# Kernel tuning notes

Hardware: AMD Instinct MI355X
Metric: run time of the kernel (lower is better)

Reference implementation:

```python
import jax, jax.numpy as jnp
import numpy as np

CD_STEPS = 1

def _sample_binary(p, u):
    # relu(sign(p - u)): 1.0 where p > u else 0.0
    return (p > u).astype(p.dtype)

def setup_inputs() -> dict:
    key = jax.random.key(0)
    k_v, k_w, k_vb, k_uh, k_uv = jax.random.split(key, 5)
    B, V, H = 8192, 2048, 1024
    return {
        "v": jax.random.uniform(k_v, (B, V), dtype=jnp.float32),
        "w": jax.random.normal(k_w, (V, H), dtype=jnp.float32) * 0.01,
        "vb": jax.random.normal(k_vb, (V,), dtype=jnp.float32) * 0.01,
        "hb": jnp.zeros((H,), dtype=jnp.float32),
        "u_h": jax.random.uniform(k_uh, (CD_STEPS + 1, B, H), dtype=jnp.float32),
        "u_v": jax.random.uniform(k_uv, (CD_STEPS, B, V), dtype=jnp.float32),
    }

def reference(v, w, vb, hb, u_h, u_v):
    sig = jax.nn.sigmoid
    # mean-field forward
    h_p = sig(hb + v @ w)                     # [B,H]
    h_prediction = h_p
    v_prediction = sig(vb + h_p @ w.T)        # [B,V]
    reconstruction_error = jnp.mean(jnp.mean(jnp.abs(v - v_prediction), axis=1))
    # data statistics
    h = _sample_binary(h_p, u_h[0])           # [B,H]
    vb_data_grad = jnp.sum(v, axis=0)
    hb_data_grad = jnp.sum(h_p, axis=0)
    # sum_b outer(v_b, h_b) == v^T @ h (original materialized [B,V,H])
    w_data_grad = jnp.einsum('bv,bh->vh', v, h)
    # CD-k chain
    vk = v
    for k in range(CD_STEPS):
        vk = _sample_binary(sig(vb + h @ w.T), u_v[k])
        h = _sample_binary(sig(hb + vk @ w), u_h[k + 1])
    vb_model_grad = jnp.sum(vk, axis=0)
    hb_model_grad = jnp.sum(h, axis=0)
    w_model_grad = jnp.einsum('bv,bh->vh', vk, h)
    vb_grad = vb_model_grad - vb_data_grad
    hb_grad = hb_model_grad - hb_data_grad
    w_grad = w_model_grad - w_data_grad
    return h_prediction, reconstruction_error, w_grad, vb_grad, hb_grad
```

## Files before the change

kernel.cpp:

```cpp
#include <hip/hip_runtime.h>


typedef unsigned short u16;
typedef short s16x8 __attribute__((ext_vector_type(8)));
typedef float f32x4 __attribute__((ext_vector_type(4)));
typedef u16 u16x4 __attribute__((ext_vector_type(4)));
typedef u16 u16x8 __attribute__((ext_vector_type(8)));

constexpr int Bn = 8192, Vn = 2048, Hn = 1024;
constexpr size_t VH = (size_t)Vn * Hn;
constexpr size_t BH = (size_t)Bn * Hn;
constexpr size_t OUT_RECON = BH;
constexpr size_t OUT_WGRAD = OUT_RECON + 1;
constexpr size_t OUT_VBG   = OUT_WGRAD + VH;
constexpr size_t OUT_HBG   = OUT_VBG + Vn;

__device__ __forceinline__ u16 f2bf(float x) {
  union { float f; unsigned u; } a; a.f = x;
  unsigned r = a.u + 0x7FFFu + ((a.u >> 16) & 1u);
  return (u16)(r >> 16);
}
__device__ __forceinline__ float bf2f(u16 h) {
  union { unsigned u; float f; } a; a.u = ((unsigned)h) << 16;
  return a.f;
}
__device__ __forceinline__ float sigmoidf_(float x) {
  return 1.0f / (1.0f + __expf(-x));
}

using gptr_t = const unsigned int __attribute__((address_space(1)))*;
using lptr_t = unsigned int __attribute__((address_space(3)))*;

__device__ __forceinline__ void gload16(const u16* g, u16* l) {
  __builtin_amdgcn_global_load_lds((gptr_t)(unsigned long long)g,
                                   (lptr_t)(unsigned long long)l, 16, 0, 0);
}

__global__ void prep_all_k(const float* __restrict__ v, u16* __restrict__ vcat,
                           u16* __restrict__ vT, float* __restrict__ vbd_p,
                           const float* __restrict__ w, u16* __restrict__ w_cat,
                           u16* __restrict__ wTc) {
  __shared__ u16 tile16[64][68];
  __shared__ float cs[16][64];
  __shared__ float tile32[64][65];
  const int bx = blockIdx.x;
  const int t = threadIdx.x;
  if (bx < 4096) {
    const int b0 = (bx & 127) << 6, c0 = (bx >> 7) << 6;
    const int rg = t >> 4;
    const int cg = (t & 15) << 2;
    float ca[4] = {0.f, 0.f, 0.f, 0.f};
#pragma unroll
    for (int i = 0; i < 4; ++i) {
      int r = rg + 16 * i;
      f32x4 x = *(const f32x4*)&v[(size_t)(b0 + r) * Vn + c0 + cg];
      u16x4 hi, lo;
#pragma unroll
      for (int j = 0; j < 4; ++j) {
        hi[j] = f2bf(x[j]);
        lo[j] = f2bf(x[j] - bf2f(hi[j]));
        tile16[r][cg + j] = hi[j];
        ca[j] += x[j];
      }
      *(u16x4*)&vcat[(size_t)(b0 + r) * (2 * Vn) + c0 + cg] = hi;
      *(u16x4*)&vcat[(size_t)(b0 + r) * (2 * Vn) + Vn + c0 + cg] = lo;
    }
#pragma unroll
    for (int j = 0; j < 4; ++j) cs[rg][cg + j] = ca[j];
    __syncthreads();
    if (t < 64) {
      float s = 0.f;
#pragma unroll
      for (int k = 0; k < 16; ++k) s += cs[k][t];
      vbd_p[(size_t)(bx & 127) * Vn + c0 + t] = s;
    }
#pragma unroll
    for (int s2 = 0; s2 < 2; ++s2) {
      int c = t >> 2;
      int seg = (t & 3) + 4 * s2;
      u16x8 pk;
#pragma unroll
      for (int i = 0; i < 8; ++i) pk[i] = tile16[seg * 8 + i][c];
      *(u16x8*)&vT[(size_t)(c0 + c) * Bn + b0 + seg * 8] = pk;
    }
  } else {
    const int wb = bx - 4096;
    const int v0 = (wb & 31) << 6, h0 = (wb >> 5) << 6;
    const int c = t & 63, r = t >> 6;
    for (int rr = r; rr < 64; rr += 4) {
      float x = w[(size_t)(v0 + rr) * Hn + h0 + c];
      tile32[rr][c] = x;
      u16 hi = f2bf(x), lo = f2bf(x - bf2f(hi));
      w_cat[(size_t)(v0 + rr) * (2 * Hn) + h0 + c]      = hi;
      w_cat[(size_t)(v0 + rr) * (2 * Hn) + Hn + h0 + c] = lo;
    }
    __syncthreads();
    for (int rr = r; rr < 64; rr += 4) {
      float x = tile32[c][rr];
      u16 hi = f2bf(x), lo = f2bf(x - bf2f(hi));
      size_t ro = (size_t)(h0 + rr) * (2 * Vn);
      wTc[ro + v0 + c]      = hi;
      wTc[ro + Vn + v0 + c] = lo;
    }
  }
}

template <int M>
__global__ void epi_h_k(const float* __restrict__ p0, const float* __restrict__ p1,
                        const float* __restrict__ bias, const float* __restrict__ uni,
                        float* __restrict__ f32out, u16* __restrict__ hp_out,
                        u16* __restrict__ hbin_out, u16* __restrict__ tout,
                        float* __restrict__ colp) {
  __shared__ u16 tile[64][68];
  __shared__ float cs[16][64];
  const int b0 = blockIdx.x * 64, c0 = blockIdx.y * 64;
  const int t = threadIdx.x;
  const int rg = t >> 4, cg = (t & 15) << 2;
  float ca[4] = {0.f, 0.f, 0.f, 0.f};
#pragma unroll
  for (int i = 0; i < 4; ++i) {
    int r = rg + 16 * i;
    size_t e = (size_t)(b0 + r) * Hn + c0 + cg;
    f32x4 a = *(const f32x4*)&p0[e];
    f32x4 b = *(const f32x4*)&p1[e];
    f32x4 uu = *(const f32x4*)&uni[e];
    f32x4 hpv;
    u16x4 hb16, qv;
#pragma unroll
    for (int j = 0; j < 4; ++j) {
      float hp = sigmoidf_(a[j] + b[j] + bias[c0 + cg + j]);
      u16 qb = (hp > uu[j]) ? (u16)0x3F80 : (u16)0;
      tile[r][cg + j] = qb;
      if constexpr (M == 1) {
        hpv[j] = hp; hb16[j] = f2bf(hp); qv[j] = qb;
        ca[j] += hp;
      } else {
        ca[j] += (qb ? 1.f : 0.f);
      }
    }
    if constexpr (M == 1) {
      *(f32x4*)&f32out[e] = hpv;
      *(u16x4*)&hp_out[e] = hb16;
      *(u16x4*)&hbin_out[e] = qv;
    }
  }
#pragma unroll
  for (int j = 0; j < 4; ++j) cs[rg][cg + j] = ca[j];
  __syncthreads();
  if (t < 64) {
    float s = 0.f;
#pragma unroll
    for (int k = 0; k < 16; ++k) s += cs[k][t];
    colp[(size_t)blockIdx.x * Hn + c0 + t] = s;
  }
#pragma unroll
  for (int s2 = 0; s2 < 2; ++s2) {
    int c = t >> 2;
    int seg = (t & 3) + 4 * s2;
    u16x8 pk;
#pragma unroll
    for (int i = 0; i < 8; ++i) pk[i] = tile[seg * 8 + i][c];
    *(u16x8*)&tout[(size_t)(c0 + c) * Bn + b0 + seg * 8] = pk;
  }
}

template <int MODE>
__global__ __launch_bounds__(512) void gemm256(
    const u16* __restrict__ A, int lda, const u16* __restrict__ Bm, int ldb, int K,
    const float* __restrict__ bias, const float* __restrict__ uni,
    const float* __restrict__ aux, float* __restrict__ f32out,
    u16* __restrict__ bfout, const u16* __restrict__ aux16,
    float* __restrict__ redp, u16* __restrict__ tout, float* __restrict__ colp) {
  constexpr bool TRANS = (MODE == 4);
  __shared__ __align__(16) u16 smem[TRANS ? 67584 : 65536];
  const int t = threadIdx.x;
  const int lane = t & 63, wave = t >> 6;
  const int wr = (wave >> 2) << 7;
  const int wc = (wave & 3) << 6;
  int bidx = blockIdx.x, bidy = blockIdx.y, bidz = blockIdx.z;
  if constexpr (MODE == 3) {
    const int orig = blockIdx.x + (blockIdx.y << 3) + (blockIdx.z << 5);
    bidz = orig & 7;
    const int r = orig >> 3;
    bidx = r & 7;
    bidy = r >> 3;
  }
  const int bm = bidx << 8, bn = bidy << 8;
  int kbeg = 0;
  float* pout = f32out;
  if constexpr (MODE == 1 || MODE == 5) {
    kbeg = bidz * K;
    pout = (bidz == 0) ? f32out : redp;
  }
  if constexpr (MODE == 3) {
    size_t off = (size_t)bidz * (size_t)K;
    A += off;
    Bm += off;
    pout = ((bidz < 4) ? f32out : redp) + (size_t)(bidz & 3) * VH;
  }
  f32x4 acc[8][4] = {};
  const int sr = t >> 2;
  const int sc = (((t & 3) ^ ((t >> 3) & 3)) << 3);
  const u16* Ag  = A  + (size_t)(bm + sr) * lda + sc;
  const u16* Ag2 = Ag + (size_t)128 * lda;
  const u16* Bg  = Bm + (size_t)(bn + sr) * ldb + sc;
  const u16* Bg2 = Bg + (size_t)128 * ldb;
  const int fr = lane & 15, fg = lane >> 4;
  const int ga = ((fg ^ ((fr >> 1) & 3)) << 3);

  auto acolf = [&](int k0) -> int {
    if constexpr (MODE == 1)      return (k0 < 2048) ? k0 : k0 - 2048;
    else if constexpr (MODE == 4) return k0 & 1023;
    else if constexpr (MODE == 5) return k0 & 2047;
    else                          return k0;
  };
  auto bcolf = [&](int k0) -> int {
    if constexpr (MODE == 1) return (k0 < 4096) ? k0 : k0 - 4096;
    else                     return k0;
  };
  auto stageA = [&](int kt) {
    const int k0 = kbeg + (kt << 5);
    const int acol = acolf(k0);
    u16* ad = smem + (kt & 3) * 8192 + wave * 512;
    gload16(Ag + acol, ad);
    gload16(Ag2 + acol, ad + 4096);
  };
  auto stageB = [&](int kt) {
    const int k0 = kbeg + (kt << 5);
    const int bcol = bcolf(k0);
    u16* bd = smem + 32768 + (kt & 3) * 8192 + wave * 512;
    gload16(Bg + bcol, bd);
    gload16(Bg2 + bcol, bd + 4096);
  };
  auto pfl4 = [&](int ci) -> float {
    const int L = (ci << 9) + t;
    return uni[(size_t)(bm + (L >> 3)) * Vn + bn + ((L & 7) << 5)];
  };

  const int NT = K >> 5;
  const int pfbeg = NT - 8;
  stageA(0); stageB(0); stageA(1); stageB(1); stageA(2); stageB(2);
  asm volatile("s_waitcnt vmcnt(8)" ::: "memory");
  __builtin_amdgcn_s_barrier();
  asm volatile("" ::: "memory");
  s16x8 bf[4], af[4];
  for (int kt = 0; kt < NT; ++kt) {
    const int pb = kt & 3;
    const u16* Ab = smem + pb * 8192;
    const u16* Bb = smem + 32768 + pb * 8192;
    const bool st = (kt < NT - 3);
#pragma unroll
    for (int n = 0; n < 4; ++n)
      bf[n] = *(const s16x8*)&Bb[(wc + n * 16 + fr) * 32 + ga];
#pragma unroll
    for (int m = 0; m < 4; ++m)
      af[m] = *(const s16x8*)&Ab[(wr + m * 16 + fr) * 32 + ga];
    if (st) stageA(kt + 3);
    if constexpr (MODE == 4) {
      if (kt >= pfbeg && kt < pfbeg + 4) {
        float pfv = pfl4(kt - pfbeg);
        asm volatile("" :: "v"(pfv));
      }
    }
    __builtin_amdgcn_s_barrier();
    asm volatile("" ::: "memory");
    __builtin_amdgcn_s_setprio(1);
#pragma unroll
    for (int m = 0; m < 4; ++m)
#pragma unroll
      for (int n = 0; n < 4; ++n)
        acc[m][n] = __builtin_amdgcn_mfma_f32_16x16x32_bf16(af[m], bf[n], acc[m][n], 0, 0, 0);
    __builtin_amdgcn_s_setprio(0);
#pragma unroll
    for (int m = 0; m < 4; ++m)
      af[m] = *(const s16x8*)&Ab[(wr + (m + 4) * 16 + fr) * 32 + ga];
    if (st) stageB(kt + 3);
    if (kt < NT - 3) {
      asm volatile("s_waitcnt vmcnt(8)" ::: "memory");
    } else if (kt == NT - 3) {
      asm volatile("s_waitcnt vmcnt(4)" ::: "memory");
    } else if (kt == NT - 2) {
      asm volatile("s_waitcnt vmcnt(0)" ::: "memory");
    }
    __builtin_amdgcn_s_barrier();
    asm volatile("" ::: "memory");
    __builtin_amdgcn_s_setprio(1);
#pragma unroll
    for (int m = 0; m < 4; ++m)
#pragma unroll
      for (int n = 0; n < 4; ++n)
        acc[m + 4][n] = __builtin_amdgcn_mfma_f32_16x16x32_bf16(af[m], bf[n], acc[m + 4][n], 0, 0, 0);
    __builtin_amdgcn_s_setprio(0);
  }

  constexpr int NC = (MODE == 4) ? Vn : Hn;
  const int fq = lane >> 4;

  if constexpr (MODE == 1 || MODE == 3 || MODE == 5) {
#pragma unroll
    for (int m = 0; m < 8; ++m)
#pragma unroll
      for (int n = 0; n < 4; ++n)
#pragma unroll
        for (int j = 0; j < 4; ++j) {
          int rl = wr + m * 16 + fq * 4 + j;
          int cl = wc + n * 16 + fr;
          pout[(size_t)(bm + rl) * NC + bn + cl] = acc[m][n][j];
        }
  }

  if constexpr (MODE == 4) {
    __syncthreads();
    float bcol[4];
#pragma unroll
    for (int n = 0; n < 4; ++n) bcol[n] = bias[bn + wc + n * 16 + fr];
    const size_t ebase = (size_t)(bm + wr + fq * 4) * NC + (bn + wc + fr);
    float ux[8][4];
    auto ld4 = [&](int ci, float* dst) {
      size_t e0 = ebase + (size_t)((ci >> 2) << 4) * NC + ((ci & 3) << 4);
      dst[0] = uni[e0];          dst[1] = uni[e0 + NC];
      dst[2] = uni[e0 + 2 * NC]; dst[3] = uni[e0 + 3 * NC];
    };
#pragma unroll
    for (int ci = 0; ci < 8; ++ci) ld4(ci, ux[ci]);
#pragma unroll
    for (int m = 0; m < 8; ++m)
#pragma unroll
      for (int n = 0; n < 4; ++n)
#pragma unroll
        for (int j = 0; j < 4; ++j)
          acc[m][n][j] = sigmoidf_(acc[m][n][j] + bcol[n]);
    float csum[4] = {0.f, 0.f, 0.f, 0.f};
#pragma unroll
    for (int ci = 0; ci < 32; ++ci) {
      const int m = ci >> 2, n = ci & 3;
      const int rl = wr + m * 16 + fq * 4;
      const int cl = wc + n * 16 + fr;
#pragma unroll
      for (int j = 0; j < 4; ++j) {
        u16 qb = (acc[m][n][j] > ux[ci & 7][j]) ? (u16)0x3F80 : (u16)0;
        smem[(rl + j) * 264 + cl] = qb;
        csum[n] += (qb ? 1.f : 0.f);
      }
      if (ci < 24) ld4(ci + 8, ux[ci & 7]);
    }
#pragma unroll
    for (int n = 0; n < 4; ++n) {
      float s = csum[n];
      s += __shfl_xor(s, 16);
      s += __shfl_xor(s, 32);
      if (fq == 0)
        colp[(size_t)(blockIdx.x * 2 + (wr >> 7)) * NC + (bn + wc + n * 16 + fr)] = s;
    }
    __syncthreads();
#pragma unroll
    for (int it = 0; it < 16; ++it) {
      int id = t + (it << 9);
      int r = id >> 5;
      int c0 = (id & 31) << 3;
      u16x8 pk = *(const u16x8*)&smem[r * 264 + c0];
      *(u16x8*)&bfout[(size_t)(bm + r) * NC + bn + c0] = pk;
    }
#pragma unroll
    for (int it = 0; it < 4; ++it) {
      int id = t + (it << 9);
      int c = id & 255;
      int q = id >> 8;
#pragma unroll
      for (int i8 = 0; i8 < 4; ++i8) {
        u16x8 pk;
#pragma unroll
        for (int i2 = 0; i2 < 8; ++i2)
          pk[i2] = smem[(q * 32 + i8 * 8 + i2) * 264 + c];
        *(u16x8*)&tout[(size_t)(bn + c) * Bn + bm + q * 32 + i8 * 8] = pk;
      }
    }
  }
}

__global__ __launch_bounds__(512) void g23_k(
    const u16* __restrict__ A2, const u16* __restrict__ B2,
    const u16* __restrict__ aux16, const float* __restrict__ bias2,
    float* __restrict__ redp2,
    const u16* __restrict__ A3, const u16* __restrict__ B3,
    float* __restrict__ out30, float* __restrict__ out34) {
  __shared__ __align__(16) u16 smem[65536];
  const int t = threadIdx.x;
  const int lane = t & 63, wave = t >> 6;
  const int wr = (wave >> 2) << 7;
  const int wc = (wave & 3) << 6;
  const int flat = blockIdx.x;
  const bool isG2 = (flat < 256);
  int bidx, bidy, bidz = 0;
  const u16 *Abase, *Bbase;
  int lda, ldb;
  if (isG2) {
    bidx = flat & 31; bidy = flat >> 5;
    Abase = A2; Bbase = B2; lda = Hn; ldb = 2 * Hn;
  } else {
    const int orig = flat - 256;
    bidz = orig & 7;
    const int rr = orig >> 3;
    bidx = rr & 7; bidy = rr >> 3;
    Abase = A3 + (size_t)bidz * 1024;
    Bbase = B3 + (size_t)bidz * 1024;
    lda = Bn; ldb = Bn;
  }
  const int bm = bidx << 8, bn = bidy << 8;
  f32x4 acc[8][4] = {};
  const int sr = t >> 2;
  const int sc = (((t & 3) ^ ((t >> 3) & 3)) << 3);
  const u16* Ag  = Abase + (size_t)(bm + sr) * lda + sc;
  const u16* Ag2 = Ag + (size_t)128 * lda;
  const u16* Bg  = Bbase + (size_t)(bn + sr) * ldb + sc;
  const u16* Bg2 = Bg + (size_t)128 * ldb;
  const int fr = lane & 15, fg = lane >> 4;
  const int ga = ((fg ^ ((fr >> 1) & 3)) << 3);

  auto stageA = [&](int kt) {
    u16* ad = smem + (kt & 3) * 8192 + wave * 512;
    gload16(Ag + (kt << 5), ad);
    gload16(Ag2 + (kt << 5), ad + 4096);
  };
  auto stageB = [&](int kt) {
    u16* bd = smem + 32768 + (kt & 3) * 8192 + wave * 512;
    gload16(Bg + (kt << 5), bd);
    gload16(Bg2 + (kt << 5), bd + 4096);
  };
  auto pfl2 = [&](int ci) -> unsigned {
    const int L = (ci << 9) + t;
    return (unsigned)aux16[(size_t)(bm + (L >> 2)) * 4096 + bn + ((L & 3) << 6)];
  };

  constexpr int NT = 32;
  stageA(0); stageB(0); stageA(1); stageB(1); stageA(2); stageB(2);
  asm volatile("s_waitcnt vmcnt(8)" ::: "memory");
  __builtin_amdgcn_s_barrier();
  asm volatile("" ::: "memory");
  s16x8 bf[4], af[4];
  for (int kt = 0; kt < NT; ++kt) {
    const int pb = kt & 3;
    const u16* Ab = smem + pb * 8192;
    const u16* Bb = smem + 32768 + pb * 8192;
    const bool st = (kt < NT - 3);
#pragma unroll
    for (int n = 0; n < 4; ++n)
      bf[n] = *(const s16x8*)&Bb[(wc + n * 16 + fr) * 32 + ga];
#pragma unroll
    for (int m = 0; m < 4; ++m)
      af[m] = *(const s16x8*)&Ab[(wr + m * 16 + fr) * 32 + ga];
    if (st) stageA(kt + 3);
    if (isG2 && kt >= NT - 8 && kt < NT - 6) {
      unsigned pfv = pfl2(kt - (NT - 8));
      asm volatile("" :: "v"(pfv));
    }
    __builtin_amdgcn_s_barrier();
    asm volatile("" ::: "memory");
    __builtin_amdgcn_s_setprio(1);
#pragma unroll
    for (int m = 0; m < 4; ++m)
#pragma unroll
      for (int n = 0; n < 4; ++n)
        acc[m][n] = __builtin_amdgcn_mfma_f32_16x16x32_bf16(af[m], bf[n], acc[m][n], 0, 0, 0);
    __builtin_amdgcn_s_setprio(0);
#pragma unroll
    for (int m = 0; m < 4; ++m)
      af[m] = *(const s16x8*)&Ab[(wr + (m + 4) * 16 + fr) * 32 + ga];
    if (st) stageB(kt + 3);
    if (kt < NT - 3) {
      asm volatile("s_waitcnt vmcnt(8)" ::: "memory");
    } else if (kt == NT - 3) {
      asm volatile("s_waitcnt vmcnt(4)" ::: "memory");
    } else if (kt == NT - 2) {
      asm volatile("s_waitcnt vmcnt(0)" ::: "memory");
    }
    __builtin_amdgcn_s_barrier();
    asm volatile("" ::: "memory");
    __builtin_amdgcn_s_setprio(1);
#pragma unroll
    for (int m = 0; m < 4; ++m)
#pragma unroll
      for (int n = 0; n < 4; ++n)
        acc[m + 4][n] = __builtin_amdgcn_mfma_f32_16x16x32_bf16(af[m], bf[n], acc[m + 4][n], 0, 0, 0);
    __builtin_amdgcn_s_setprio(0);
  }

  const int fq = lane >> 4;
  if (isG2) {
    float bcol[4];
#pragma unroll
    for (int n = 0; n < 4; ++n) bcol[n] = bias2[bn + wc + n * 16 + fr];
    const size_t ebase = (size_t)(bm + wr + fq * 4) * 4096 + (bn + wc + fr);
    float ax[8][4];
    auto ld4 = [&](int ci, float* dst) {
      size_t e0 = ebase + (size_t)((ci >> 2) << 4) * 4096 + ((ci & 3) << 4);
      dst[0] = bf2f(aux16[e0]);            dst[1] = bf2f(aux16[e0 + 4096]);
      dst[2] = bf2f(aux16[e0 + 2 * 4096]); dst[3] = bf2f(aux16[e0 + 3 * 4096]);
    };
#pragma unroll
    for (int ci = 0; ci < 8; ++ci) ld4(ci, ax[ci]);
#pragma unroll
    for (int m = 0; m < 8; ++m)
#pragma unroll
      for (int n = 0; n < 4; ++n)
#pragma unroll
        for (int j = 0; j < 4; ++j)
          acc[m][n][j] = sigmoidf_(acc[m][n][j] + bcol[n]);
    float lsum = 0.f;
#pragma unroll
    for (int ci = 0; ci < 32; ++ci) {
      const int m = ci >> 2, n = ci & 3;
#pragma unroll
      for (int j = 0; j < 4; ++j) lsum += fabsf(ax[ci & 7][j] - acc[m][n][j]);
      if (ci < 24) ld4(ci + 8, ax[ci & 7]);
    }
#pragma unroll
    for (int off = 32; off > 0; off >>= 1) lsum += __shfl_down(lsum, off);
    __syncthreads();
    float* redlds = (float*)smem;
    if (lane == 0) redlds[wave] = lsum;
    __syncthreads();
    if (t == 0) {
      float s = 0.f;
#pragma unroll
      for (int wv = 0; wv < 8; ++wv) s += redlds[wv];
      redp2[(size_t)bidy * 32 + bidx] = s;
    }
  } else {
    float* pout = ((bidz < 4) ? out30 : out34) + (size_t)(bidz & 3) * VH;
#pragma unroll
    for (int m = 0; m < 8; ++m)
#pragma unroll
      for (int n = 0; n < 4; ++n)
#pragma unroll
        for (int j = 0; j < 4; ++j) {
          int rl = wr + m * 16 + fq * 4 + j;
          int cl = wc + n * 16 + fr;
          pout[(size_t)(bm + rl) * Hn + bn + cl] = acc[m][n][j];
        }
  }
}

__global__ void reduce8_k(const float* __restrict__ p, float* __restrict__ out) {
  size_t e = ((size_t)blockIdx.x * 256 + threadIdx.x) * 4;
  f32x4 r = {};
#pragma unroll
  for (int z = 0; z < 8; ++z) r += *(const f32x4*)&p[(size_t)z * VH + e];
  out[e + 0] = r[0]; out[e + 1] = r[1]; out[e + 2] = r[2]; out[e + 3] = r[3];
}

__global__ void tail_k(const float* __restrict__ pa, const float* __restrict__ pb,
                       const float* __restrict__ sums, float* __restrict__ out) {
  const int b = blockIdx.x;
  float* outw = out + OUT_WGRAD;
  if (b < 2048) {
    size_t e = ((size_t)b * 256 + threadIdx.x) * 4;
    f32x4 r = {};
#pragma unroll
    for (int z = 0; z < 4; ++z) r += *(const f32x4*)&pa[(size_t)z * VH + e];
#pragma unroll
    for (int z = 0; z < 4; ++z) r += *(const f32x4*)&pb[(size_t)z * VH + e];
    float s0 = outw[e + 0], s1 = outw[e + 1], s2 = outw[e + 2], s3 = outw[e + 3];
    outw[e + 0] = r[0] - s0; outw[e + 1] = r[1] - s1;
    outw[e + 2] = r[2] - s2; outw[e + 3] = r[3] - s3;
  } else {
    const int i = (b - 2048) * 256 + threadIdx.x;
    const float* recon_p = sums;
    const float* vbd = sums + 1024;
    const float* hbd = vbd + 128 * 2048;
    const float* vbm = hbd + 128 * 1024;
    const float* hbm = vbm + 128 * 2048;
    if (i < 2048) {
      float d = 0.f, m = 0.f;
      for (int k = 0; k < 128; ++k) d += vbd[k * 2048 + i];
      for (int k = 0; k < 64; ++k)  m += vbm[k * 2048 + i];
      out[OUT_VBG + i] = m - d;
    }
    if (i < 1024) {
      float d = 0.f, m = 0.f;
      for (int k = 0; k < 128; ++k) { d += hbd[k * 1024 + i]; m += hbm[k * 1024 + i]; }
      out[OUT_HBG + i] = m - d;
    }
    if (i == 0) {
      float s = 0.f;
      for (int k = 0; k < 256; ++k) s += recon_p[k];
      out[OUT_RECON] = s * (1.0f / 16777216.0f);
    }
  }
}

extern "C" void kernel_launch(void* const* d_in, const int* in_sizes, int n_in,
                              void* d_out, int out_size, void* d_ws, size_t ws_size,
                              hipStream_t stream) {
  (void)in_sizes; (void)n_in; (void)out_size;
  const float* v   = (const float*)d_in[0];
  const float* w   = (const float*)d_in[1];
  const float* vb  = (const float*)d_in[2];
  const float* hb  = (const float*)d_in[3];
  const float* u_h = (const float*)d_in[4];
  const float* u_v = (const float*)d_in[5];
  float* out = (float*)d_out;
  char* ws = (char*)d_ws;
  if (ws_size < 204734464ULL) return;

  float* sums    = (float*)ws;
  float* recon_p = sums;
  float* vbd_p   = sums + 1024;
  float* hbd_p   = vbd_p + 128 * 2048;
  float* vbm_p   = hbd_p + 128 * 1024;
  float* hbm_p   = vbm_p + 128 * 2048;
  char* p = ws + 3407872;
  u16* v_cat  = (u16*)p;  p += (size_t)Bn * 2 * Vn * 2;
  u16* wT_cat = (u16*)p;  p += (size_t)Hn * 2 * Vn * 2;
  u16* w_cat  = (u16*)p;  p += (size_t)Vn * 2 * Hn * 2;
  u16* h_p    = (u16*)p;  p += BH * 2;
  u16* hbin   = (u16*)p;  p += BH * 2;
  u16* vT     = (u16*)p;  p += (size_t)Vn * Bn * 2;
  u16* hT     = (u16*)p;  p += (size_t)Hn * Bn * 2;
  float* big  = (float*)p;
  u16* vk   = v_cat;
  u16* vkT  = vT;
  u16* h2T  = hT;
  float* vcat_f = (float*)v_cat;
  float* hpbuf  = (float*)h_p;
  float* outW   = out + OUT_WGRAD;

  prep_all_k<<<4608, 256, 0, stream>>>(v, v_cat, vT, vbd_p, w, w_cat, wT_cat);
  gemm256<1><<<dim3(32, 4, 2), 512, 0, stream>>>(
      v_cat, 2 * Vn, wT_cat, 2 * Vn, 3072, nullptr, nullptr, nullptr,
      out, nullptr, nullptr, big, nullptr, nullptr);
  epi_h_k<1><<<dim3(128, 16), 256, 0, stream>>>(
      out, big, hb, u_h, out, h_p, hbin, hT, hbd_p);
  g23_k<<<512, 512, 0, stream>>>(
      h_p, w_cat, v_cat, vb, recon_p,
      vT, hT, vcat_f, vcat_f + 4 * VH);
  reduce8_k<<<2048, 256, 0, stream>>>(vcat_f, outW);
  gemm256<4><<<dim3(32, 8), 512, 0, stream>>>(
      hbin, Hn, w_cat, 2 * Hn, 2 * Hn, vb, u_v, nullptr,
      nullptr, vk, nullptr, nullptr, vkT, vbm_p);
  gemm256<5><<<dim3(32, 4, 2), 512, 0, stream>>>(
      vk, Vn, wT_cat, 2 * Vn, 2048, nullptr, nullptr, nullptr,
      hpbuf, nullptr, nullptr, big, nullptr, nullptr);
  epi_h_k<5><<<dim3(128, 16), 256, 0, stream>>>(
      hpbuf, big, hb, u_h + BH, nullptr, nullptr, nullptr, h2T, hbm_p);
  gemm256<3><<<dim3(Vn / 256, Hn / 256, 8), 512, 0, stream>>>(
      vkT, Bn, h2T, Bn, 1024, nullptr, nullptr, nullptr,
      hpbuf, nullptr, nullptr, big, nullptr, nullptr);
  tail_k<<<2056, 256, 0, stream>>>(hpbuf, big, sums, out);
}
```

Measured before the change: 493.8 us.

## Compute binary model-gradient GEMM with int8 MFMA on byte-packed transposes

The model-statistics GEMM (vk^T @ h) works only on 0/1 operands, so the epilogues that write vkT and h2T now emit 8-bit values instead of bf16. A new int8 MFMA kernel (16x16x64) with a 4-stage LDS pipeline and split-K over 8 slices replaces the bf16 gemm256<3>. Exact integer accumulation preserves correctness while halving operand bytes and using the higher-throughput int8 matrix path. The added cost is a new hand-scheduled kernel with explicit waitcnt and barrier logic.

Result: faster. 479.7 us (-2.9%).

```diff
diff --git a/kernel.cpp b/kernel.cpp
--- a/kernel.cpp
+++ b/kernel.cpp
@@ -2,10 +2,13 @@
 
 
 typedef unsigned short u16;
+typedef unsigned char u8;
 typedef short s16x8 __attribute__((ext_vector_type(8)));
 typedef float f32x4 __attribute__((ext_vector_type(4)));
+typedef int i32x4 __attribute__((ext_vector_type(4)));
 typedef u16 u16x4 __attribute__((ext_vector_type(4)));
 typedef u16 u16x8 __attribute__((ext_vector_type(8)));
+typedef u8 u8x8 __attribute__((ext_vector_type(8)));
 
 constexpr int Bn = 8192, Vn = 2048, Hn = 1024;
 constexpr size_t VH = (size_t)Vn * Hn;
@@ -31,7 +34,7 @@
 using gptr_t = const unsigned int __attribute__((address_space(1)))*;
 using lptr_t = unsigned int __attribute__((address_space(3)))*;
 
-__device__ __forceinline__ void gload16(const u16* g, u16* l) {
+__device__ __forceinline__ void gload16(const void* g, void* l) {
   __builtin_amdgcn_global_load_lds((gptr_t)(unsigned long long)g,
                                    (lptr_t)(unsigned long long)l, 16, 0, 0);
 }
@@ -153,14 +156,27 @@
     for (int k = 0; k < 16; ++k) s += cs[k][t];
     colp[(size_t)blockIdx.x * Hn + c0 + t] = s;
   }
-#pragma unroll
-  for (int s2 = 0; s2 < 2; ++s2) {
-    int c = t >> 2;
-    int seg = (t & 3) + 4 * s2;
-    u16x8 pk;
-#pragma unroll
-    for (int i = 0; i < 8; ++i) pk[i] = tile[seg * 8 + i][c];
-    *(u16x8*)&tout[(size_t)(c0 + c) * Bn + b0 + seg * 8] = pk;
+  if constexpr (M == 5) {
+    u8* tout8 = (u8*)tout;
+#pragma unroll
+    for (int s2 = 0; s2 < 2; ++s2) {
+      int c = t >> 2;
+      int seg = (t & 3) + 4 * s2;
+      u8x8 pk;
+#pragma unroll
+      for (int i = 0; i < 8; ++i) pk[i] = tile[seg * 8 + i][c] ? (u8)1 : (u8)0;
+      *(u8x8*)&tout8[(size_t)(c0 + c) * Bn + b0 + seg * 8] = pk;
+    }
+  } else {
+#pragma unroll
+    for (int s2 = 0; s2 < 2; ++s2) {
+      int c = t >> 2;
+      int seg = (t & 3) + 4 * s2;
+      u16x8 pk;
+#pragma unroll
+      for (int i = 0; i < 8; ++i) pk[i] = tile[seg * 8 + i][c];
+      *(u16x8*)&tout[(size_t)(c0 + c) * Bn + b0 + seg * 8] = pk;
+    }
   }
 }
 
@@ -361,21 +377,117 @@
       u16x8 pk = *(const u16x8*)&smem[r * 264 + c0];
       *(u16x8*)&bfout[(size_t)(bm + r) * NC + bn + c0] = pk;
     }
-#pragma unroll
-    for (int it = 0; it < 4; ++it) {
-      int id = t + (it << 9);
-      int c = id & 255;
-      int q = id >> 8;
-#pragma unroll
-      for (int i8 = 0; i8 < 4; ++i8) {
-        u16x8 pk;
+    {
+      u8* tout8 = (u8*)tout;
+      const int c = t & 255;
+      const int half = t >> 8;
+#pragma unroll
+      for (int i8_ = 0; i8_ < 16; ++i8_) {
+        u8x8 pk;
 #pragma unroll
         for (int i2 = 0; i2 < 8; ++i2)
-          pk[i2] = smem[(q * 32 + i8 * 8 + i2) * 264 + c];
-        *(u16x8*)&tout[(size_t)(bn + c) * Bn + bm + q * 32 + i8 * 8] = pk;
+          pk[i2] = smem[(half * 128 + i8_ * 8 + i2) * 264 + c] ? (u8)1 : (u8)0;
+        *(u8x8*)&tout8[(size_t)(bn + c) * Bn + bm + half * 128 + i8_ * 8] = pk;
       }
     }
   }
+}
+
+__global__ __launch_bounds__(512) void gemm_i8_k(
+    const u8* __restrict__ A, const u8* __restrict__ Bm,
+    float* __restrict__ out0, float* __restrict__ out4) {
+  __shared__ __align__(16) u8 smem[131072];
+  const int t = threadIdx.x;
+  const int lane = t & 63, wave = t >> 6;
+  const int wr = (wave >> 2) << 7;
+  const int wc = (wave & 3) << 6;
+  const int orig = blockIdx.x + (blockIdx.y << 3) + (blockIdx.z << 5);
+  const int bidz = orig & 7;
+  const int rr = orig >> 3;
+  const int bidx = rr & 7, bidy = rr >> 3;
+  const int bm = bidx << 8, bn = bidy << 8;
+  const int kbeg = bidz << 10;
+  float* pout = ((bidz < 4) ? out0 : out4) + (size_t)(bidz & 3) * VH;
+  i32x4 acc[8][4] = {};
+  const int sr = t >> 2;
+  const int sc = (((t & 3) ^ ((t >> 3) & 3)) << 4);
+  const u8* Ag  = A  + (size_t)(bm + sr) * Bn + sc;
+  const u8* Ag2 = Ag + (size_t)128 * Bn;
+  const u8* Bg  = Bm + (size_t)(bn + sr) * Bn + sc;
+  const u8* Bg2 = Bg + (size_t)128 * Bn;
+  const int fr = lane & 15, fg = lane >> 4;
+  const int ga = ((fg ^ ((fr >> 1) & 3)) << 4);
+
+  auto stageA = [&](int kt) {
+    u8* ad = smem + (kt & 3) * 16384 + wave * 1024;
+    gload16(Ag + kbeg + (kt << 6), ad);
+    gload16(Ag2 + kbeg + (kt << 6), ad + 8192);
+  };
+  auto stageB = [&](int kt) {
+    u8* bd = smem + 65536 + (kt & 3) * 16384 + wave * 1024;
+    gload16(Bg + kbeg + (kt << 6), bd);
+    gload16(Bg2 + kbeg + (kt << 6), bd + 8192);
+  };
+
+  constexpr int NT = 16;
+  stageA(0); stageB(0); stageA(1); stageB(1); stageA(2); stageB(2);
+  asm volatile("s_waitcnt vmcnt(8)" ::: "memory");
+  __builtin_amdgcn_s_barrier();
+  asm volatile("" ::: "memory");
+  i32x4 bf[4], af[4];
+  for (int kt = 0; kt < NT; ++kt) {
+    const u8* Ab = smem + (kt & 3) * 16384;
+    const u8* Bb = smem + 65536 + (kt & 3) * 16384;
+    const bool st = (kt < NT - 3);
+#pragma unroll
+    for (int n = 0; n < 4; ++n)
+      bf[n] = *(const i32x4*)&Bb[(wc + n * 16 + fr) * 64 + ga];
+#pragma unroll
+    for (int m = 0; m < 4; ++m)
+      af[m] = *(const i32x4*)&Ab[(wr + m * 16 + fr) * 64 + ga];
+    if (st) stageA(kt + 3);
+    __builtin_amdgcn_s_barrier();
+    asm volatile("" ::: "memory");
+    __builtin_amdgcn_s_setprio(1);
+#pragma unroll
+    for (int m = 0; m < 4; ++m)
+#pragma unroll
+      for (int n = 0; n < 4; ++n)
+        acc[m][n] = __builtin_amdgcn_mfma_i32_16x16x64_i8(af[m], bf[n], acc[m][n], 0, 0, 0);
+    __builtin_amdgcn_s_setprio(0);
+#pragma unroll
+    for (int m = 0; m < 4; ++m)
+      af[m] = *(const i32x4*)&Ab[(wr + (m + 4) * 16 + fr) * 64 + ga];
+    if (st) stageB(kt + 3);
+    if (kt < NT - 3) {
+      asm volatile("s_waitcnt vmcnt(8)" ::: "memory");
+    } else if (kt == NT - 3) {
+      asm volatile("s_waitcnt vmcnt(4)" ::: "memory");
+    } else if (kt == NT - 2) {
+      asm volatile("s_waitcnt vmcnt(0)" ::: "memory");
+    }
+    __builtin_amdgcn_s_barrier();
+    asm volatile("" ::: "memory");
+    __builtin_amdgcn_s_setprio(1);
+#pragma unroll
+    for (int m = 0; m < 4; ++m)
+#pragma unroll
+      for (int n = 0; n < 4; ++n)
+        acc[m + 4][n] = __builtin_amdgcn_mfma_i32_16x16x64_i8(af[m], bf[n], acc[m + 4][n], 0, 0, 0);
+    __builtin_amdgcn_s_setprio(0);
+  }
+
+  const int fq = lane >> 4;
+#pragma unroll
+  for (int m = 0; m < 8; ++m)
+#pragma unroll
+    for (int n = 0; n < 4; ++n)
+#pragma unroll
+      for (int j = 0; j < 4; ++j) {
+        int rl = wr + m * 16 + fq * 4 + j;
+        int cl = wc + n * 16 + fr;
+        pout[(size_t)(bm + rl) * Hn + bn + cl] = (float)acc[m][n][j];
+      }
 }
 
 __global__ __launch_bounds__(512) void g23_k(
@@ -619,8 +731,8 @@
   u16* hT     = (u16*)p;  p += (size_t)Hn * Bn * 2;
   float* big  = (float*)p;
   u16* vk   = v_cat;
-  u16* vkT  = vT;
-  u16* h2T  = hT;
+  u8*  vkT8 = (u8*)vT;
+  u8*  h2T8 = (u8*)hT;
   float* vcat_f = (float*)v_cat;
   float* hpbuf  = (float*)h_p;
   float* outW   = out + OUT_WGRAD;
@@ -637,14 +749,12 @@
   reduce8_k<<<2048, 256, 0, stream>>>(vcat_f, outW);
   gemm256<4><<<dim3(32, 8), 512, 0, stream>>>(
       hbin, Hn, w_cat, 2 * Hn, 2 * Hn, vb, u_v, nullptr,
-      nullptr, vk, nullptr, nullptr, vkT, vbm_p);
+      nullptr, vk, nullptr, nullptr, (u16*)vkT8, vbm_p);
   gemm256<5><<<dim3(32, 4, 2), 512, 0, stream>>>(
       vk, Vn, wT_cat, 2 * Vn, 2048, nullptr, nullptr, nullptr,
       hpbuf, nullptr, nullptr, big, nullptr, nullptr);
   epi_h_k<5><<<dim3(128, 16), 256, 0, stream>>>(
-      hpbuf, big, hb, u_h + BH, nullptr, nullptr, nullptr, h2T, hbm_p);
-  gemm256<3><<<dim3(Vn / 256, Hn / 256, 8), 512, 0, stream>>>(
-      vkT, Bn, h2T, Bn, 1024, nullptr, nullptr, nullptr,
-      hpbuf, nullptr, nullptr, big, nullptr, nullptr);
+      hpbuf, big, hb, u_h + BH, nullptr, nullptr, nullptr, (u16*)h2T8, hbm_p);
+  gemm_i8_k<<<dim3(8, 4, 8), 512, 0, stream>>>(vkT8, h2T8, hpbuf, big);
   tail_k<<<2056, 256, 0, stream>>>(hpbuf, big, sums, out);
 }
```
